# Kernel tuning notes

Measured on AMD Instinct MI355X. Metric: run time of the kernel, lower is better.

## Reference

```python
import jax, jax.numpy as jnp
import numpy as np

B, S, H, NH = 2, 2048, 1024, 16
HD = H // NH  # 64
BASE = 10000.0


def _rope_tables(seq_len, head_dim):
    inv_freq = 1.0 / (BASE ** (jnp.arange(0, head_dim, 2, dtype=jnp.float32) / head_dim))
    t = jnp.arange(seq_len, dtype=jnp.float32)
    freqs = jnp.outer(t, inv_freq)            # [S, HD/2]
    emb = jnp.concatenate([freqs, freqs], -1)  # [S, HD]
    return jnp.cos(emb), jnp.sin(emb)


def _rotate_half(x):
    x1, x2 = jnp.split(x, 2, axis=-1)
    return jnp.concatenate([-x2, x1], axis=-1)


def setup_inputs() -> dict:
    key = jax.random.key(0)
    ks = jax.random.split(key, 5)
    sc = 1.0 / np.sqrt(H)
    return {
        "hidden_states": jax.random.normal(ks[0], (B, S, H), jnp.float32),
        "Wq": jax.random.normal(ks[1], (H, H), jnp.float32) * sc,
        "Wk": jax.random.normal(ks[2], (H, H), jnp.float32) * sc,
        "Wv": jax.random.normal(ks[3], (H, H), jnp.float32) * sc,
        "Wo": jax.random.normal(ks[4], (H, H), jnp.float32) * sc,
    }


def reference(hidden_states, Wq, Wk, Wv, Wo):
    b, s, h = hidden_states.shape
    # nn.Linear: y = x @ W.T
    q = hidden_states @ Wq.T
    k = hidden_states @ Wk.T
    v = hidden_states @ Wv.T
    # [B, NH, S, HD]
    q = q.reshape(b, s, NH, HD).transpose(0, 2, 1, 3)
    k = k.reshape(b, s, NH, HD).transpose(0, 2, 1, 3)
    v = v.reshape(b, s, NH, HD).transpose(0, 2, 1, 3)
    cos, sin = _rope_tables(s, HD)  # [S, HD], broadcast over B, NH
    q = q * cos + _rotate_half(q) * sin
    k = k * cos + _rotate_half(k) * sin
    scores = jnp.einsum('bhqd,bhkd->bhqk', q, k) / jnp.sqrt(jnp.float32(HD))
    probs = jax.nn.softmax(scores, axis=-1)
    ctx = jnp.einsum('bhqk,bhkd->bhqd', probs, v)
    ctx = ctx.transpose(0, 2, 1, 3).reshape(b, s, h)
    return ctx @ Wo.T
```

## Files before the change

### kernel.cpp

```cpp
#include <hip/hip_runtime.h>
#include <hip/hip_bf16.h>
#include <math.h>

typedef __hip_bfloat16 bf16;
typedef float f32x4 __attribute__((ext_vector_type(4)));
typedef float f32x16 __attribute__((ext_vector_type(16)));
typedef short s16x8 __attribute__((ext_vector_type(8)));

#define NB 2
#define SEQ 2048
#define HID 1024
#define NHEAD 16
#define HD 64
#define BH (NB * NHEAD)
#define MROWS (NB * SEQ)
#define QSCL 0.18033688011111793f

static __device__ __forceinline__ f32x4 mfma16(s16x8 a, s16x8 b, f32x4 c) {
  return __builtin_amdgcn_mfma_f32_16x16x32_bf16(a, b, c, 0, 0, 0);
}
static __device__ __forceinline__ f32x16 mfma32(s16x8 a, s16x8 b, f32x16 c) {
  return __builtin_amdgcn_mfma_f32_32x32x16_bf16(a, b, c, 0, 0, 0);
}

static __device__ __forceinline__ void gload_lds16(const bf16* g, bf16* l) {
  __builtin_amdgcn_global_load_lds((const __attribute__((address_space(1))) void*)g,
                                   (__attribute__((address_space(3))) void*)l, 16, 0, 0);
}

static __device__ __forceinline__ unsigned pack_bf16(float a, float b) {
  __hip_bfloat162 t = __float22bfloat162_rn(float2{a, b});
  return *(unsigned*)&t;
}

__global__ __launch_bounds__(256) void prep_kernel(const float* __restrict__ X,
                                                   const float* __restrict__ wq, const float* __restrict__ wk,
                                                   const float* __restrict__ wv, const float* __restrict__ wo,
                                                   bf16* __restrict__ Xb, bf16* __restrict__ wqkv,
                                                   bf16* __restrict__ wob,
                                                   float* __restrict__ ct, float* __restrict__ st) {
  int bid = blockIdx.x, tid = threadIdx.x;
  if (bid < 8192) {
    const float* src;
    bf16* dst;
    int i;
    if (bid < 4096) {
      src = X; dst = Xb;
      i = (bid * 256 + tid) * 4;
    } else {
      int wsel = (bid - 4096) >> 10;
      src = (wsel == 0) ? wq : (wsel == 1) ? wk : (wsel == 2) ? wv : wo;
      dst = (wsel < 3) ? (wqkv + (size_t)wsel * HID * HID) : wob;
      i = (((bid - 4096) & 1023) * 256 + tid) * 4;
    }
    float4 v = *(const float4*)(src + i);
    bf16 a0 = __float2bfloat16(v.x), a1 = __float2bfloat16(v.y);
    bf16 a2 = __float2bfloat16(v.z), a3 = __float2bfloat16(v.w);
    ushort4 u;
    u.x = *(const unsigned short*)&a0;
    u.y = *(const unsigned short*)&a1;
    u.z = *(const unsigned short*)&a2;
    u.w = *(const unsigned short*)&a3;
    *(ushort4*)(dst + i) = u;
  } else {
    int i = (bid - 8192) * 256 + tid;
    int s = i >> 5, j = i & 31;
    float inv = expf(-(float)(2 * j) * (9.210340371976184f / 64.0f));
    float ang = (float)s * inv;
    float sn, cs;
    sincosf(ang, &sn, &cs);
    ct[i] = cs;
    st[i] = sn;
  }
}

template <int MODE>
__global__ __launch_bounds__(256) void gemm_bt(const bf16* __restrict__ A, const bf16* __restrict__ Bm,
                                               float* __restrict__ C,
                                               bf16* __restrict__ Qb, bf16* __restrict__ Kb,
                                               bf16* __restrict__ Vtg,
                                               const float* __restrict__ ct, const float* __restrict__ st,
                                               int M, int N, int K) {
  __shared__ __align__(16) bf16 As[128][32];
  __shared__ __align__(16) bf16 Bs[128][32];
  const int tid = threadIdx.x, lane = tid & 63, wid = tid >> 6;
  const int wm = wid >> 1, wn = wid & 1;
  const int tm = blockIdx.y * 128, tn = blockIdx.x * 128;
  const int lrow = lane >> 2;
  const int lcol = (lane & 3) * 8;

  f32x4 acc[4][4];
#pragma unroll
  for (int i = 0; i < 4; ++i)
#pragma unroll
    for (int j = 0; j < 4; ++j) acc[i][j] = (f32x4){0.f, 0.f, 0.f, 0.f};

  for (int k0 = 0; k0 < K; k0 += 32) {
    __syncthreads();
    {
      int r0 = wid * 32;
      gload_lds16(A  + (size_t)(tm + r0 +      lrow) * K + k0 + lcol, &As[r0][0]);
      gload_lds16(A  + (size_t)(tm + r0 + 16 + lrow) * K + k0 + lcol, &As[r0 + 16][0]);
      gload_lds16(Bm + (size_t)(tn + r0 +      lrow) * K + k0 + lcol, &Bs[r0][0]);
      gload_lds16(Bm + (size_t)(tn + r0 + 16 + lrow) * K + k0 + lcol, &Bs[r0 + 16][0]);
    }
    __syncthreads();
    s16x8 af[4], bfr[4];
#pragma unroll
    for (int mi = 0; mi < 4; ++mi)
      af[mi] = *(const s16x8*)&As[wm * 64 + mi * 16 + (lane & 15)][(lane >> 4) * 8];
#pragma unroll
    for (int ni = 0; ni < 4; ++ni)
      bfr[ni] = *(const s16x8*)&Bs[wn * 64 + ni * 16 + (lane & 15)][(lane >> 4) * 8];
#pragma unroll
    for (int mi = 0; mi < 4; ++mi)
#pragma unroll
      for (int ni = 0; ni < 4; ++ni)
        acc[mi][ni] = mfma16(af[mi], bfr[ni], acc[mi][ni]);
  }

  if (MODE == 0) {
    const int tblk = tn >> 10;
    if (tblk < 2) {
      const float scl = (tblk == 0) ? QSCL : 1.0f;
#pragma unroll
      for (int mi = 0; mi < 4; ++mi) {
#pragma unroll
        for (int r = 0; r < 4; ++r) {
          int row = tm + wm * 64 + mi * 16 + (lane >> 4) * 4 + r;
          int s = row & (SEQ - 1);
#pragma unroll
          for (int p = 0; p < 2; ++p) {
            int j = p * 16 + (lane & 15);
            float c = ct[s * 32 + j], sn = st[s * 32 + j];
            float x0 = acc[mi][p][r], x1 = acc[mi][p + 2][r];
            acc[mi][p][r]     = (x0 * c - x1 * sn) * scl;
            acc[mi][p + 2][r] = (x1 * c + x0 * sn) * scl;
          }
        }
      }
    }
  }

#pragma unroll
  for (int mi = 0; mi < 4; ++mi) {
#pragma unroll
    for (int ni = 0; ni < 4; ++ni) {
#pragma unroll
      for (int r = 0; r < 4; ++r) {
        int row = tm + wm * 64 + mi * 16 + (lane >> 4) * 4 + r;
        int col = tn + wn * 64 + ni * 16 + (lane & 15);
        float v = acc[mi][ni][r];
        if (MODE == 0) {
          int t = col >> 10, c = col & (HID - 1);
          int h = c >> 6, d = c & 63;
          int b = row >> 11, s = row & (SEQ - 1);
          size_t bh = (size_t)(b * NHEAD + h);
          if (t == 0)      Qb[(bh * SEQ + s) * HD + d]  = __float2bfloat16(v);
          else if (t == 1) Kb[(bh * SEQ + s) * HD + d]  = __float2bfloat16(v);
          else             Vtg[(bh * HD + d) * SEQ + s] = __float2bfloat16(v);
        } else {
          C[(size_t)row * N + col] = v;
        }
      }
    }
  }
}

__global__ __launch_bounds__(512, 4) void attn_kernel(const bf16* __restrict__ Q, const bf16* __restrict__ K,
                                                      const bf16* __restrict__ Vt, bf16* __restrict__ ctx) {
  __shared__ __align__(16) bf16 S[32768];
  const int tid = threadIdx.x, l = tid & 63, w = tid >> 6;
  const int lq = l & 31, hi = l >> 5;
  const int grp = w >> 2, wq = w & 3;
  const int gtid = tid & 255;

  const int id = blockIdx.x;
  const int lin = (id & 7) * 64 + (id >> 3);
  const int bh = lin >> 4, qb = lin & 15;

  const bf16* Qp  = Q  + ((size_t)bh * SEQ + qb * 128) * HD;
  const bf16* Kp0 = K  + (size_t)bh * SEQ * HD;
  const bf16* Vp0 = Vt + (size_t)bh * HD * SEQ;

  bf16* Ksg = S + grp * 16384;
  bf16* Vsg = S + grp * 16384 + 8192;

  s16x8 qf[4];
  {
    const bf16* qr = Qp + (wq * 32 + lq) * HD + hi * 8;
#pragma unroll
    for (int ks = 0; ks < 4; ++ks) qf[ks] = *(const s16x8*)(qr + ks * 16);
  }

  const int s0 = gtid, s1 = gtid + 256;
  const int R0 = s0 >> 3, R1 = s1 >> 3;
  const int c0 = ((s0 & 7) ^ (R0 & 7)) * 8;
  const int c1 = ((s1 & 7) ^ (R1 & 7)) * 8;
  const int p0 = (R0 & 51) | ((R0 & 4) << 1) | ((R0 & 8) >> 1);
  const int p1 = (R1 & 51) | ((R1 & 4) << 1) | ((R1 & 8) >> 1);
  const bf16* kS0 = Kp0 + p0 * HD + c0;
  const bf16* kS1 = Kp0 + p1 * HD + c1;
  const bf16* vS0 = Vp0 + (size_t)R0 * SEQ + c0;
  const bf16* vS1 = Vp0 + (size_t)R1 * SEQ + c1;

#define STAGE(t, b)                                                 \
  do {                                                              \
    gload_lds16(kS0 + (size_t)(t) * (64 * HD), Ksg + (b) * 4096 + s0 * 8); \
    gload_lds16(kS1 + (size_t)(t) * (64 * HD), Ksg + (b) * 4096 + s1 * 8); \
    gload_lds16(vS0 + (t) * 64,                Vsg + (b) * 4096 + s0 * 8); \
    gload_lds16(vS1 + (t) * 64,                Vsg + (b) * 4096 + s1 * 8); \
  } while (0)

  STAGE(grp * 16, 0);
  __syncthreads();

  float m_run = -INFINITY, lsum = 0.f;
  f32x16 acc0{}, acc1{};

  const int NSTEP = 16;
  for (int i = 0; i < NSTEP; ++i) {
    const int cur = i & 1;
    if (i + 1 < NSTEP) STAGE(grp * 16 + i + 1, cur ^ 1);
    const bf16* Kc = Ksg + cur * 4096;
    const bf16* Vc = Vsg + cur * 4096;

    f32x16 sf0{}, sf1{};
    __builtin_amdgcn_s_setprio(1);
#pragma unroll
    for (int ks = 0; ks < 4; ++ks) {
      const int slot = (ks * 2 + hi) ^ (lq & 7);
      sf0 = mfma32(*(const s16x8*)(Kc + lq * 64 + slot * 8),        qf[ks], sf0);
      sf1 = mfma32(*(const s16x8*)(Kc + (32 + lq) * 64 + slot * 8), qf[ks], sf1);
    }
    __builtin_amdgcn_s_setprio(0);

    float pmax = sf0[0];
#pragma unroll
    for (int i2 = 1; i2 < 16; ++i2) pmax = fmaxf(pmax, sf0[i2]);
#pragma unroll
    for (int i2 = 0; i2 < 16; ++i2) pmax = fmaxf(pmax, sf1[i2]);
    pmax = fmaxf(pmax, __shfl_xor(pmax, 32));

    if (__any(pmax > m_run + 8.f)) {
      float mn = fmaxf(m_run, pmax);
      float corr = __builtin_amdgcn_exp2f(m_run - mn);
      m_run = mn;
      lsum *= corr;
#pragma unroll
      for (int r = 0; r < 16; ++r) {
        float cr = __shfl(corr, (r & 3) + 8 * (r >> 2) + 4 * hi);
        acc0[r] *= cr;
        acc1[r] *= cr;
      }
    }

    float ls = 0.f;
#pragma unroll
    for (int i2 = 0; i2 < 16; ++i2) {
      sf0[i2] = __builtin_amdgcn_exp2f(sf0[i2] - m_run);
      ls += sf0[i2];
    }
#pragma unroll
    for (int i2 = 0; i2 < 16; ++i2) {
      sf1[i2] = __builtin_amdgcn_exp2f(sf1[i2] - m_run);
      ls += sf1[i2];
    }
    lsum += ls;

    s16x8 pf[4];
#pragma unroll
    for (int kt = 0; kt < 4; ++kt) {
      union { unsigned u[4]; s16x8 v; } cc;
#pragma unroll
      for (int vv = 0; vv < 4; ++vv) {
        if (kt < 2) cc.u[vv] = pack_bf16(sf0[(kt & 1) * 8 + 2 * vv], sf0[(kt & 1) * 8 + 2 * vv + 1]);
        else        cc.u[vv] = pack_bf16(sf1[(kt & 1) * 8 + 2 * vv], sf1[(kt & 1) * 8 + 2 * vv + 1]);
      }
      pf[kt] = cc.v;
    }

    __builtin_amdgcn_s_setprio(1);
#pragma unroll
    for (int kt = 0; kt < 4; ++kt) {
      const int slot = (kt * 2 + hi) ^ (lq & 7);
      acc0 = mfma32(pf[kt], *(const s16x8*)(Vc + lq * 64 + slot * 8),        acc0);
      acc1 = mfma32(pf[kt], *(const s16x8*)(Vc + (32 + lq) * 64 + slot * 8), acc1);
    }
    __builtin_amdgcn_s_setprio(0);
    __syncthreads();
  }
#undef STAGE

  lsum += __shfl_xor(lsum, 32);

  float* Op = (float*)(S + 16384);
  float* Mp = (float*)(S);
  float* Lp = Mp + 128;

  if (grp == 1) {
    if (hi == 0) {
      Mp[wq * 32 + lq] = m_run;
      Lp[wq * 32 + lq] = lsum;
    }
#pragma unroll
    for (int r = 0; r < 16; ++r) {
      int q = (r & 3) + 8 * (r >> 2) + 4 * hi;
      Op[(wq * 32 + q) * 64 + lq]      = acc0[r];
      Op[(wq * 32 + q) * 64 + 32 + lq] = acc1[r];
    }
  }
  __syncthreads();

  if (grp == 0) {
    float m1 = Mp[wq * 32 + lq], l1 = Lp[wq * 32 + lq];
    float mN = fmaxf(m_run, m1);
    float cr0 = __builtin_amdgcn_exp2f(m_run - mN);
    float cr1 = __builtin_amdgcn_exp2f(m1 - mN);
    float inv = 1.0f / (lsum * cr0 + l1 * cr1);

    const int b = bh >> 4, h = bh & (NHEAD - 1);
#pragma unroll
    for (int r = 0; r < 16; ++r) {
      int q = (r & 3) + 8 * (r >> 2) + 4 * hi;
      float c0q = __shfl(cr0, q);
      float c1q = __shfl(cr1, q);
      float invq = __shfl(inv, q);
      float o0 = (acc0[r] * c0q + Op[(wq * 32 + q) * 64 + lq]      * c1q) * invq;
      float o1 = (acc1[r] * c0q + Op[(wq * 32 + q) * 64 + 32 + lq] * c1q) * invq;
      size_t base = ((size_t)b * SEQ + qb * 128 + wq * 32 + q) * HID + h * HD + lq;
      ctx[base]      = __float2bfloat16(o0);
      ctx[base + 32] = __float2bfloat16(o1);
    }
  }
}

extern "C" void kernel_launch(void* const* d_in, const int* in_sizes, int n_in,
                              void* d_out, int out_size, void* d_ws, size_t ws_size,
                              hipStream_t stream) {
  const float* X  = (const float*)d_in[0];
  const float* Wq = (const float*)d_in[1];
  const float* Wk = (const float*)d_in[2];
  const float* Wv = (const float*)d_in[3];
  const float* Wo = (const float*)d_in[4];

  char* p = (char*)d_ws;
  bf16* Xb   = (bf16*)p; p += (size_t)MROWS * HID * 2;
  bf16* Wqkv = (bf16*)p; p += (size_t)3 * HID * HID * 2;
  bf16* Wob  = (bf16*)p; p += (size_t)HID * HID * 2;
  bf16* Qb   = (bf16*)p; p += (size_t)BH * SEQ * HD * 2;
  bf16* Kb   = (bf16*)p; p += (size_t)BH * SEQ * HD * 2;
  bf16* Vtg  = (bf16*)p; p += (size_t)BH * HD * SEQ * 2;
  bf16* Cb   = (bf16*)p; p += (size_t)MROWS * HID * 2;
  float* ct  = (float*)p; p += (size_t)SEQ * 32 * 4;
  float* st  = (float*)p; p += (size_t)SEQ * 32 * 4;

  prep_kernel<<<8448, 256, 0, stream>>>(X, Wq, Wk, Wv, Wo, Xb, Wqkv, Wob, ct, st);

  gemm_bt<0><<<dim3(3 * HID / 128, MROWS / 128), 256, 0, stream>>>(
      Xb, Wqkv, nullptr, Qb, Kb, Vtg, ct, st, MROWS, 3 * HID, HID);

  attn_kernel<<<dim3(512), 512, 0, stream>>>(Qb, Kb, Vtg, Cb);

  gemm_bt<1><<<dim3(HID / 128, MROWS / 128), 256, 0, stream>>>(
      Cb, Wob, (float*)d_out, nullptr, nullptr, nullptr, nullptr, nullptr, MROWS, HID, HID);
}
```

Baseline: 138.0 us.

## Use explicit vmcnt waits with split barriers and tree reductions in attention loop

Replaces the full __syncthreads at the loop end with an explicit barrier / stage-next-tile / s_waitcnt vmcnt(4) / barrier sequence, so only the current tile's async LDS loads must land before compute. The prefetch of the next tile can stay in flight across the barrier. It also rewrites the row-max and row-sum reductions as pairwise trees to shorten the dependency chains. The risk is that the hand-tuned vmcnt count is tied to the exact number of loads per stage.

```diff
diff --git a/kernel.cpp b/kernel.cpp
--- a/kernel.cpp
+++ b/kernel.cpp
@@ -213,15 +213,23 @@
   } while (0)
 
   STAGE(grp * 16, 0);
-  __syncthreads();
 
   float m_run = -INFINITY, lsum = 0.f;
   f32x16 acc0{}, acc1{};
 
   const int NSTEP = 16;
-  for (int i = 0; i < NSTEP; ++i) {
-    const int cur = i & 1;
-    if (i + 1 < NSTEP) STAGE(grp * 16 + i + 1, cur ^ 1);
+  for (int t = 0; t < NSTEP; ++t) {
+    const int cur = t & 1;
+    __builtin_amdgcn_s_barrier();
+    if (t + 1 < NSTEP) {
+      STAGE(grp * 16 + t + 1, cur ^ 1);
+      asm volatile("s_waitcnt vmcnt(4)" ::: "memory");
+    } else {
+      asm volatile("s_waitcnt vmcnt(0)" ::: "memory");
+    }
+    __builtin_amdgcn_sched_barrier(0);
+    __builtin_amdgcn_s_barrier();
+
     const bf16* Kc = Ksg + cur * 4096;
     const bf16* Vc = Vsg + cur * 4096;
 
@@ -235,12 +243,15 @@
     }
     __builtin_amdgcn_s_setprio(0);
 
-    float pmax = sf0[0];
-#pragma unroll
-    for (int i2 = 1; i2 < 16; ++i2) pmax = fmaxf(pmax, sf0[i2]);
-#pragma unroll
-    for (int i2 = 0; i2 < 16; ++i2) pmax = fmaxf(pmax, sf1[i2]);
-    pmax = fmaxf(pmax, __shfl_xor(pmax, 32));
+    float mx[16];
+#pragma unroll
+    for (int i = 0; i < 16; ++i) mx[i] = fmaxf(sf0[i], sf1[i]);
+#pragma unroll
+    for (int w2 = 8; w2 >= 1; w2 >>= 1)
+#pragma unroll
+      for (int i = 0; i < 8; ++i)
+        if (i < w2) mx[i] = fmaxf(mx[i], mx[i + w2]);
+    float pmax = fmaxf(mx[0], __shfl_xor(mx[0], 32));
 
     if (__any(pmax > m_run + 8.f)) {
       float mn = fmaxf(m_run, pmax);
@@ -255,18 +266,19 @@
       }
     }
 
-    float ls = 0.f;
-#pragma unroll
-    for (int i2 = 0; i2 < 16; ++i2) {
-      sf0[i2] = __builtin_amdgcn_exp2f(sf0[i2] - m_run);
-      ls += sf0[i2];
-    }
-#pragma unroll
-    for (int i2 = 0; i2 < 16; ++i2) {
-      sf1[i2] = __builtin_amdgcn_exp2f(sf1[i2] - m_run);
-      ls += sf1[i2];
-    }
-    lsum += ls;
+#pragma unroll
+    for (int i = 0; i < 16; ++i) sf0[i] = __builtin_amdgcn_exp2f(sf0[i] - m_run);
+#pragma unroll
+    for (int i = 0; i < 16; ++i) sf1[i] = __builtin_amdgcn_exp2f(sf1[i] - m_run);
+    float sm[16];
+#pragma unroll
+    for (int i = 0; i < 16; ++i) sm[i] = sf0[i] + sf1[i];
+#pragma unroll
+    for (int w2 = 8; w2 >= 1; w2 >>= 1)
+#pragma unroll
+      for (int i = 0; i < 8; ++i)
+        if (i < w2) sm[i] += sm[i + w2];
+    lsum += sm[0];
 
     s16x8 pf[4];
 #pragma unroll
@@ -288,11 +300,12 @@
       acc1 = mfma32(pf[kt], *(const s16x8*)(Vc + (32 + lq) * 64 + slot * 8), acc1);
     }
     __builtin_amdgcn_s_setprio(0);
-    __syncthreads();
   }
 #undef STAGE
 
   lsum += __shfl_xor(lsum, 32);
+
+  __syncthreads();
 
   float* Op = (float*)(S + 16384);
   float* Mp = (float*)(S);
```

After: 138.2 us. About the same (+0.1%).

## Deepen attention K/V pipeline to four LDS buffers and process two tiles per iteration

Applied to the files above, without the earlier changes.

The attention kernel doubles LDS to hold four K/V stages per group and prefetches two tiles ahead, using explicit vmcnt waits and raw barriers in place of a full __syncthreads each step. Each loop iteration now handles two 64-key tiles, with the QK MFMAs for both issued back to back. The softmax max and sum reductions become tree reductions to shorten dependency chains. In exchange, launch bounds drop from 4 to 2 blocks per SM and LDS use doubles, which cuts occupancy.

```diff
diff --git a/kernel.cpp b/kernel.cpp
--- a/kernel.cpp
+++ b/kernel.cpp
@@ -167,9 +167,9 @@
   }
 }
 
-__global__ __launch_bounds__(512, 4) void attn_kernel(const bf16* __restrict__ Q, const bf16* __restrict__ K,
+__global__ __launch_bounds__(512, 2) void attn_kernel(const bf16* __restrict__ Q, const bf16* __restrict__ K,
                                                       const bf16* __restrict__ Vt, bf16* __restrict__ ctx) {
-  __shared__ __align__(16) bf16 S[32768];
+  __shared__ __align__(16) bf16 S[65536];
   const int tid = threadIdx.x, l = tid & 63, w = tid >> 6;
   const int lq = l & 31, hi = l >> 5;
   const int grp = w >> 2, wq = w & 3;
@@ -183,8 +183,8 @@
   const bf16* Kp0 = K  + (size_t)bh * SEQ * HD;
   const bf16* Vp0 = Vt + (size_t)bh * HD * SEQ;
 
-  bf16* Ksg = S + grp * 16384;
-  bf16* Vsg = S + grp * 16384 + 8192;
+  bf16* Ksg = S + grp * 32768;
+  bf16* Vsg = S + grp * 32768 + 16384;
 
   s16x8 qf[4];
   {
@@ -204,97 +204,122 @@
   const bf16* vS0 = Vp0 + (size_t)R0 * SEQ + c0;
   const bf16* vS1 = Vp0 + (size_t)R1 * SEQ + c1;
 
-#define STAGE(t, b)                                                 \
-  do {                                                              \
+#define STAGE(t, b)                                                        \
+  do {                                                                     \
     gload_lds16(kS0 + (size_t)(t) * (64 * HD), Ksg + (b) * 4096 + s0 * 8); \
     gload_lds16(kS1 + (size_t)(t) * (64 * HD), Ksg + (b) * 4096 + s1 * 8); \
     gload_lds16(vS0 + (t) * 64,                Vsg + (b) * 4096 + s0 * 8); \
     gload_lds16(vS1 + (t) * 64,                Vsg + (b) * 4096 + s1 * 8); \
   } while (0)
 
-  STAGE(grp * 16, 0);
-  __syncthreads();
+  const int base = grp * 16;
+  STAGE(base + 0, 0);
+  STAGE(base + 1, 1);
 
   float m_run = -INFINITY, lsum = 0.f;
   f32x16 acc0{}, acc1{};
 
-  const int NSTEP = 16;
-  for (int i = 0; i < NSTEP; ++i) {
-    const int cur = i & 1;
-    if (i + 1 < NSTEP) STAGE(grp * 16 + i + 1, cur ^ 1);
-    const bf16* Kc = Ksg + cur * 4096;
-    const bf16* Vc = Vsg + cur * 4096;
-
-    f32x16 sf0{}, sf1{};
+#define PROCESS(sf0, sf1, pf)                                                        \
+  do {                                                                               \
+    float mx[16];                                                                    \
+    _Pragma("unroll") for (int i = 0; i < 16; ++i) mx[i] = fmaxf(sf0[i], sf1[i]);    \
+    _Pragma("unroll") for (int w2 = 8; w2 >= 1; w2 >>= 1)                            \
+      _Pragma("unroll") for (int i = 0; i < 8; ++i)                                  \
+        if (i < w2) mx[i] = fmaxf(mx[i], mx[i + w2]);                                \
+    float pmax = fmaxf(mx[0], __shfl_xor(mx[0], 32));                                \
+    if (__any(pmax > m_run + 8.f)) {                                                 \
+      float mn = fmaxf(m_run, pmax);                                                 \
+      float corr = __builtin_amdgcn_exp2f(m_run - mn);                               \
+      m_run = mn;                                                                    \
+      lsum *= corr;                                                                  \
+      _Pragma("unroll") for (int r = 0; r < 16; ++r) {                               \
+        float cr = __shfl(corr, (r & 3) + 8 * (r >> 2) + 4 * hi);                    \
+        acc0[r] *= cr;                                                               \
+        acc1[r] *= cr;                                                               \
+      }                                                                              \
+    }                                                                                \
+    _Pragma("unroll") for (int i = 0; i < 16; ++i) sf0[i] = __builtin_amdgcn_exp2f(sf0[i] - m_run); \
+    _Pragma("unroll") for (int i = 0; i < 16; ++i) sf1[i] = __builtin_amdgcn_exp2f(sf1[i] - m_run); \
+    float sm[16];                                                                    \
+    _Pragma("unroll") for (int i = 0; i < 16; ++i) sm[i] = sf0[i] + sf1[i];          \
+    _Pragma("unroll") for (int w2 = 8; w2 >= 1; w2 >>= 1)                            \
+      _Pragma("unroll") for (int i = 0; i < 8; ++i)                                  \
+        if (i < w2) sm[i] += sm[i + w2];                                             \
+    lsum += sm[0];                                                                   \
+    _Pragma("unroll") for (int kt = 0; kt < 4; ++kt) {                               \
+      union { unsigned u[4]; s16x8 v; } cc;                                          \
+      _Pragma("unroll") for (int vv = 0; vv < 4; ++vv) {                             \
+        if (kt < 2) cc.u[vv] = pack_bf16(sf0[(kt & 1) * 8 + 2 * vv], sf0[(kt & 1) * 8 + 2 * vv + 1]); \
+        else        cc.u[vv] = pack_bf16(sf1[(kt & 1) * 8 + 2 * vv], sf1[(kt & 1) * 8 + 2 * vv + 1]); \
+      }                                                                              \
+      pf[kt] = cc.v;                                                                 \
+    }                                                                                \
+  } while (0)
+
+  for (int ss = 0; ss < 8; ++ss) {
+    const int bufA = (ss & 1) * 2, bufB = bufA + 1;
+    __builtin_amdgcn_s_barrier();
+    if (ss < 7) {
+      STAGE(base + 2 * ss + 2, (bufA + 2) & 3);
+      STAGE(base + 2 * ss + 3, (bufB + 2) & 3);
+      asm volatile("s_waitcnt vmcnt(8)" ::: "memory");
+    } else {
+      asm volatile("s_waitcnt vmcnt(0)" ::: "memory");
+    }
+    __builtin_amdgcn_sched_barrier(0);
+    __builtin_amdgcn_s_barrier();
+
+    const bf16* KcA = Ksg + bufA * 4096;
+    const bf16* VcA = Vsg + bufA * 4096;
+    const bf16* KcB = Ksg + bufB * 4096;
+    const bf16* VcB = Vsg + bufB * 4096;
+
+    f32x16 sA0{}, sA1{}, sB0{}, sB1{};
     __builtin_amdgcn_s_setprio(1);
 #pragma unroll
     for (int ks = 0; ks < 4; ++ks) {
       const int slot = (ks * 2 + hi) ^ (lq & 7);
-      sf0 = mfma32(*(const s16x8*)(Kc + lq * 64 + slot * 8),        qf[ks], sf0);
-      sf1 = mfma32(*(const s16x8*)(Kc + (32 + lq) * 64 + slot * 8), qf[ks], sf1);
+      sA0 = mfma32(*(const s16x8*)(KcA + lq * 64 + slot * 8),        qf[ks], sA0);
+      sA1 = mfma32(*(const s16x8*)(KcA + (32 + lq) * 64 + slot * 8), qf[ks], sA1);
+    }
+#pragma unroll
+    for (int ks = 0; ks < 4; ++ks) {
+      const int slot = (ks * 2 + hi) ^ (lq & 7);
+      sB0 = mfma32(*(const s16x8*)(KcB + lq * 64 + slot * 8),        qf[ks], sB0);
+      sB1 = mfma32(*(const s16x8*)(KcB + (32 + lq) * 64 + slot * 8), qf[ks], sB1);
     }
     __builtin_amdgcn_s_setprio(0);
 
-    float pmax = sf0[0];
-#pragma unroll
-    for (int i2 = 1; i2 < 16; ++i2) pmax = fmaxf(pmax, sf0[i2]);
-#pragma unroll
-    for (int i2 = 0; i2 < 16; ++i2) pmax = fmaxf(pmax, sf1[i2]);
-    pmax = fmaxf(pmax, __shfl_xor(pmax, 32));
-
-    if (__any(pmax > m_run + 8.f)) {
-      float mn = fmaxf(m_run, pmax);
-      float corr = __builtin_amdgcn_exp2f(m_run - mn);
-      m_run = mn;
-      lsum *= corr;
-#pragma unroll
-      for (int r = 0; r < 16; ++r) {
-        float cr = __shfl(corr, (r & 3) + 8 * (r >> 2) + 4 * hi);
-        acc0[r] *= cr;
-        acc1[r] *= cr;
-      }
-    }
-
-    float ls = 0.f;
-#pragma unroll
-    for (int i2 = 0; i2 < 16; ++i2) {
-      sf0[i2] = __builtin_amdgcn_exp2f(sf0[i2] - m_run);
-      ls += sf0[i2];
-    }
-#pragma unroll
-    for (int i2 = 0; i2 < 16; ++i2) {
-      sf1[i2] = __builtin_amdgcn_exp2f(sf1[i2] - m_run);
-      ls += sf1[i2];
-    }
-    lsum += ls;
-
-    s16x8 pf[4];
-#pragma unroll
-    for (int kt = 0; kt < 4; ++kt) {
-      union { unsigned u[4]; s16x8 v; } cc;
-#pragma unroll
-      for (int vv = 0; vv < 4; ++vv) {
-        if (kt < 2) cc.u[vv] = pack_bf16(sf0[(kt & 1) * 8 + 2 * vv], sf0[(kt & 1) * 8 + 2 * vv + 1]);
-        else        cc.u[vv] = pack_bf16(sf1[(kt & 1) * 8 + 2 * vv], sf1[(kt & 1) * 8 + 2 * vv + 1]);
-      }
-      pf[kt] = cc.v;
-    }
-
+    s16x8 pfA[4];
+    PROCESS(sA0, sA1, pfA);
     __builtin_amdgcn_s_setprio(1);
 #pragma unroll
     for (int kt = 0; kt < 4; ++kt) {
       const int slot = (kt * 2 + hi) ^ (lq & 7);
-      acc0 = mfma32(pf[kt], *(const s16x8*)(Vc + lq * 64 + slot * 8),        acc0);
-      acc1 = mfma32(pf[kt], *(const s16x8*)(Vc + (32 + lq) * 64 + slot * 8), acc1);
+      acc0 = mfma32(pfA[kt], *(const s16x8*)(VcA + lq * 64 + slot * 8),        acc0);
+      acc1 = mfma32(pfA[kt], *(const s16x8*)(VcA + (32 + lq) * 64 + slot * 8), acc1);
     }
     __builtin_amdgcn_s_setprio(0);
-    __syncthreads();
+
+    s16x8 pfB[4];
+    PROCESS(sB0, sB1, pfB);
+    __builtin_amdgcn_s_setprio(1);
+#pragma unroll
+    for (int kt = 0; kt < 4; ++kt) {
+      const int slot = (kt * 2 + hi) ^ (lq & 7);
+      acc0 = mfma32(pfB[kt], *(const s16x8*)(VcB + lq * 64 + slot * 8),        acc0);
+      acc1 = mfma32(pfB[kt], *(const s16x8*)(VcB + (32 + lq) * 64 + slot * 8), acc1);
+    }
+    __builtin_amdgcn_s_setprio(0);
   }
 #undef STAGE
+#undef PROCESS
 
   lsum += __shfl_xor(lsum, 32);
 
-  float* Op = (float*)(S + 16384);
+  __syncthreads();
+
+  float* Op = (float*)(S + 32768);
   float* Mp = (float*)(S);
   float* Lp = Mp + 128;
 
@@ -328,9 +353,9 @@
       float invq = __shfl(inv, q);
       float o0 = (acc0[r] * c0q + Op[(wq * 32 + q) * 64 + lq]      * c1q) * invq;
       float o1 = (acc1[r] * c0q + Op[(wq * 32 + q) * 64 + 32 + lq] * c1q) * invq;
-      size_t base = ((size_t)b * SEQ + qb * 128 + wq * 32 + q) * HID + h * HD + lq;
-      ctx[base]      = __float2bfloat16(o0);
-      ctx[base + 32] = __float2bfloat16(o1);
+      size_t base2 = ((size_t)b * SEQ + qb * 128 + wq * 32 + q) * HID + h * HD + lq;
+      ctx[base2]      = __float2bfloat16(o0);
+      ctx[base2 + 32] = __float2bfloat16(o1);
     }
   }
 }
```

New measurement: 145.6 us. 5.5% more time.
